# Optimization experiments

Hardware: AMD Instinct MI355X
Metric: run time of the kernel (lower is better)

## Reference

```python
import jax, jax.numpy as jnp
import numpy as np

H = 3          # num_hops + 1
N = 16384      # nodes per hop (seq len after view(1, -1, d))
D_MODEL = 256
D_STATE = 16
D_CONV = 8
EXPAND = 2
D_INNER = EXPAND * D_MODEL  # 512
DT_RANK = (D_MODEL + 15) // 16  # 16


def setup_inputs() -> dict:
    key = jax.random.key(0)
    ks = jax.random.split(key, 10)
    s = 0.02
    h = jax.random.normal(ks[0], (H, N, D_MODEL), jnp.float32)
    in_proj_w = jax.random.normal(ks[1], (H, 2 * D_INNER, D_MODEL), jnp.float32) * s
    conv_w = jax.random.normal(ks[2], (H, D_INNER, D_CONV), jnp.float32) * s
    conv_b = jax.random.normal(ks[3], (H, D_INNER), jnp.float32) * s
    x_proj_w = jax.random.normal(ks[4], (H, DT_RANK + 2 * D_STATE, D_INNER), jnp.float32) * s
    dt_proj_w = jax.random.normal(ks[5], (H, D_INNER, DT_RANK), jnp.float32) * s
    # dt bias so that softplus(dt_bias) is a small positive step (mamba-style init)
    dt_proj_b = jax.random.uniform(ks[6], (H, D_INNER), jnp.float32, minval=-5.0, maxval=-2.0)
    # A_log init: A = [1..d_state] broadcast over channels (S4D-real init)
    A_log = jnp.log(jnp.tile(jnp.arange(1, D_STATE + 1, dtype=jnp.float32), (H, D_INNER, 1)))
    D_skip = jnp.ones((H, D_INNER), jnp.float32)
    out_proj_w = jax.random.normal(ks[7], (H, D_MODEL, D_INNER), jnp.float32) * s
    return {
        "h": h, "in_proj_w": in_proj_w, "conv_w": conv_w, "conv_b": conv_b,
        "x_proj_w": x_proj_w, "dt_proj_w": dt_proj_w, "dt_proj_b": dt_proj_b,
        "A_log": A_log, "D_skip": D_skip, "out_proj_w": out_proj_w,
    }


def _mamba_one_hop(h, ipw, cw, cb, xpw, dtw, dtb, A_log, Dp, opw):
    # h: [N, d_model] -- seq len N, batch 1 (squeezed)
    xz = h @ ipw.T                              # [N, 2*d_inner]
    x, z = jnp.split(xz, 2, axis=-1)            # each [N, d_inner]
    # causal depthwise conv1d (left pad d_conv-1, truncate to N)
    xp = jnp.pad(x, ((D_CONV - 1, 0), (0, 0)))
    xc = cb + sum(cw[:, k] * xp[k:k + N] for k in range(D_CONV))  # [N, d_inner]
    u = jax.nn.silu(xc)
    # input-dependent dt, B, C
    x_dbl = u @ xpw.T                           # [N, dt_rank + 2*d_state]
    dt = x_dbl[:, :DT_RANK]
    Bm = x_dbl[:, DT_RANK:DT_RANK + D_STATE]    # [N, d_state]
    Cm = x_dbl[:, DT_RANK + D_STATE:]           # [N, d_state]
    delta = jax.nn.softplus(dt @ dtw.T + dtb)   # [N, d_inner]
    A = -jnp.exp(A_log)                         # [d_inner, d_state]

    def step(state, inp):
        d_t, b_t, c_t, u_t = inp                # [d_inner],[d_state],[d_state],[d_inner]
        dA = jnp.exp(d_t[:, None] * A)          # [d_inner, d_state]
        state = dA * state + (d_t * u_t)[:, None] * b_t[None, :]
        y_t = jnp.sum(state * c_t[None, :], axis=-1)  # [d_inner]
        return state, y_t

    state0 = jnp.zeros((D_INNER, D_STATE), h.dtype)
    _, y = jax.lax.scan(step, state0, (delta, Bm, Cm, u))  # y: [N, d_inner]
    y = y + u * Dp
    y = y * jax.nn.silu(z)
    return y @ opw.T                            # [N, d_model]


def reference(h, in_proj_w, conv_w, conv_b, x_proj_w, dt_proj_w, dt_proj_b,
              A_log, D_skip, out_proj_w):
    # vmap over the (num_hops+1) independent Mamba blocks
    return jax.vmap(_mamba_one_hop)(h, in_proj_w, conv_w, conv_b, x_proj_w,
                                    dt_proj_w, dt_proj_b, A_log, D_skip, out_proj_w)
```

## Files before the change

kernel.cpp:

```cpp
#include <hip/hip_runtime.h>

#define N_SEQ   16384
#define DM      256
#define DI      512
#define DS      16
#define DTR     16
#define NCHUNK  256
#define CHUNK   64
#define NSEG    8
#define SEGLEN  32

typedef short bf16x8 __attribute__((ext_vector_type(8)));
typedef float f32x4  __attribute__((ext_vector_type(4)));

__device__ __forceinline__ float b2f(ushort u){
  union { unsigned int i; float f; } v; v.i = ((unsigned int)u) << 16; return v.f;
}
__device__ __forceinline__ ushort f2b(float f){
  union { float f; unsigned int i; } v; v.f = f;
  unsigned int r = v.i + 0x7fffu + ((v.i >> 16) & 1u);
  return (ushort)(r >> 16);
}
__device__ __forceinline__ float silu_f(float x){
  return x * __builtin_amdgcn_rcpf(1.f + __expf(-x));
}
__device__ __forceinline__ void async16(const ushort* g, short* l){
  __builtin_amdgcn_global_load_lds(
      (const __attribute__((address_space(1))) unsigned int*)g,
      (__attribute__((address_space(3))) unsigned int*)l, 16, 0, 0);
}

__global__ __launch_bounds__(256) void cvt_kernel(const float* __restrict__ src,
                                                  ushort* __restrict__ dst, int n){
  int i = (blockIdx.x * 256 + threadIdx.x) * 4;
  if (i >= n) return;
  float4 v = *(const float4*)(src + i);
  ushort4 o;
  o.x = f2b(v.x); o.y = f2b(v.y); o.z = f2b(v.z); o.w = f2b(v.w);
  *(ushort4*)(dst + i) = o;
}

template<int BM, int BN, int WAR, int WWR, int MODE>
__global__ __launch_bounds__(256) void gemm2(const ushort* __restrict__ A,
                                             const ushort* __restrict__ W,
                                             int M, int Nn, int K,
                                             void* __restrict__ out0,
                                             void* __restrict__ out1, int ldc){
  constexpr int AI = WAR / 16, WI = WWR / 16;
  constexpr int WROWS = BM / WAR;
  constexpr int SMEM_STAGE = (BM + BN) * 64 * 2;
  constexpr int SMEM_EPI   = (MODE == 0) ? BM * (BN + 8) * 2 : 0;
  constexpr int SMEM = SMEM_STAGE > SMEM_EPI ? SMEM_STAGE : SMEM_EPI;
  __shared__ char smem[SMEM];
  short* As = (short*)smem;
  short* Ws = As + BM * 64;

  const int tid = threadIdx.x, lane = tid & 63, wid = tid >> 6;
  const int bz = blockIdx.z;
  const int rowBase = blockIdx.x * BM, colBase = blockIdx.y * BN;
  const ushort* Ah = A + (size_t)bz * M * K + (size_t)rowBase * K;
  const ushort* Wh = W + (size_t)bz * Nn * K + (size_t)colBase * K;
  const int wmi = wid % WROWS, wni = wid / WROWS;
  const int lr = lane & 15, q = lane >> 4;
  const int srow = lane >> 3, scg = lane & 7;

  f32x4 acc[AI][WI];
  #pragma unroll
  for (int ai = 0; ai < AI; ai++)
    #pragma unroll
    for (int wi = 0; wi < WI; wi++)
      acc[ai][wi] = (f32x4){0.f, 0.f, 0.f, 0.f};

  for (int kt = 0; kt < K; kt += 64){
    #pragma unroll
    for (int wdx = wid; wdx < BM / 8; wdx += 4){
      int r = wdx * 8 + srow;
      async16(Ah + (size_t)r * K + kt + ((scg ^ (r & 7)) * 8), As + wdx * 512);
    }
    #pragma unroll
    for (int wdx = wid; wdx < BN / 8; wdx += 4){
      int r = wdx * 8 + srow;
      async16(Wh + (size_t)r * K + kt + ((scg ^ (r & 7)) * 8), Ws + wdx * 512);
    }
    __syncthreads();
    #pragma unroll
    for (int ks = 0; ks < 64; ks += 32){
      bf16x8 wf[WI], af[AI];
      #pragma unroll
      for (int wi = 0; wi < WI; wi++){
        int row = wni * WWR + wi * 16 + lr;
        int pg = ((ks >> 3) + q) ^ (row & 7);
        wf[wi] = *(const bf16x8*)&Ws[row * 64 + pg * 8];
      }
      #pragma unroll
      for (int ai = 0; ai < AI; ai++){
        int row = wmi * WAR + ai * 16 + lr;
        int pg = ((ks >> 3) + q) ^ (row & 7);
        af[ai] = *(const bf16x8*)&As[row * 64 + pg * 8];
      }
      #pragma unroll
      for (int ai = 0; ai < AI; ai++)
        #pragma unroll
        for (int wi = 0; wi < WI; wi++)
          acc[ai][wi] = __builtin_amdgcn_mfma_f32_16x16x32_bf16(wf[wi], af[ai], acc[ai][wi], 0, 0, 0);
    }
    __syncthreads();
  }

  if (MODE == 0){
    const bool isz = (colBase >= DI);
    short* Cl = (short*)smem;
    constexpr int LDC = BN + 8;
    #pragma unroll
    for (int ai = 0; ai < AI; ai++){
      #pragma unroll
      for (int wi = 0; wi < WI; wi++){
        int trow = wmi * WAR + ai * 16 + lr;
        int tcol = wni * WWR + wi * 16 + q * 4;
        ushort4 pk;
        float v0 = acc[ai][wi][0], v1 = acc[ai][wi][1], v2 = acc[ai][wi][2], v3 = acc[ai][wi][3];
        if (isz){ v0 = silu_f(v0); v1 = silu_f(v1); v2 = silu_f(v2); v3 = silu_f(v3); }
        pk.x = f2b(v0); pk.y = f2b(v1); pk.z = f2b(v2); pk.w = f2b(v3);
        *(ushort4*)&Cl[trow * LDC + tcol] = pk;
      }
    }
    __syncthreads();
    ushort* dst = isz ? (ushort*)out1 : (ushort*)out0;
    const int colx = isz ? colBase - DI : colBase;
    const int rr = tid >> 4, ch = tid & 15;
    #pragma unroll
    for (int i = 0; i < BM / 16; i++){
      int trow = i * 16 + rr;
      uint4 v = *(uint4*)&Cl[trow * LDC + ch * 8];
      *(uint4*)(dst + ((size_t)bz * M + rowBase + trow) * DI + colx + ch * 8) = v;
    }
  } else {
    float* o = (float*)out0;
    #pragma unroll
    for (int ai = 0; ai < AI; ai++){
      #pragma unroll
      for (int wi = 0; wi < WI; wi++){
        int row = rowBase + wmi * WAR + ai * 16 + lr;
        int col = colBase + wni * WWR + wi * 16 + q * 4;
        *(float4*)&o[((size_t)bz * M + row) * ldc + col] = *(float4*)&acc[ai][wi];
      }
    }
  }
}

__global__ __launch_bounds__(256) void conv_kernel(const ushort* __restrict__ x_bf,
                                                   const float* __restrict__ cw,
                                                   const float* __restrict__ cb,
                                                   ushort* __restrict__ u_bf){
  const int SEG = 128;
  const int hop = blockIdx.z;
  const int c0 = threadIdx.x * 2;
  const int t0 = blockIdx.x * SEG;
  float k0[8], k1[8];
  {
    const float* r0 = cw + (size_t)(hop * DI + c0) * 8;
    float4 a = *(const float4*)r0, b = *(const float4*)(r0 + 4);
    k0[0]=a.x;k0[1]=a.y;k0[2]=a.z;k0[3]=a.w;k0[4]=b.x;k0[5]=b.y;k0[6]=b.z;k0[7]=b.w;
    float4 c = *(const float4*)(r0 + 8), d = *(const float4*)(r0 + 12);
    k1[0]=c.x;k1[1]=c.y;k1[2]=c.z;k1[3]=c.w;k1[4]=d.x;k1[5]=d.y;k1[6]=d.z;k1[7]=d.w;
  }
  float2 bias = *(const float2*)(cb + hop * DI + c0);
  const int rb = hop * N_SEQ;
  float w0[7], w1[7];
  #pragma unroll
  for (int j = 0; j < 7; j++){
    int t = t0 - 7 + j;
    if (t >= 0){
      ushort2 xv = *(const ushort2*)&x_bf[(size_t)(rb + t) * DI + c0];
      w0[j] = b2f(xv.x); w1[j] = b2f(xv.y);
    } else { w0[j] = 0.f; w1[j] = 0.f; }
  }
  #pragma unroll 4
  for (int tt = 0; tt < SEG; tt++){
    ushort2 xv = *(const ushort2*)&x_bf[(size_t)(rb + t0 + tt) * DI + c0];
    float x0 = b2f(xv.x), x1 = b2f(xv.y);
    float a0 = fmaf(k0[7], x0, bias.x), a1 = fmaf(k1[7], x1, bias.y);
    #pragma unroll
    for (int j = 0; j < 7; j++){ a0 = fmaf(k0[j], w0[j], a0); a1 = fmaf(k1[j], w1[j], a1); }
    ushort2 o; o.x = f2b(silu_f(a0)); o.y = f2b(silu_f(a1));
    *(ushort2*)&u_bf[(size_t)(rb + t0 + tt) * DI + c0] = o;
    #pragma unroll
    for (int j = 0; j < 6; j++){ w0[j] = w0[j + 1]; w1[j] = w1[j + 1]; }
    w0[6] = x0; w1[6] = x1;
  }
}

__global__ __launch_bounds__(256) void dtd_kernel(const float* __restrict__ xdbl,
                                                  const float* __restrict__ dtw,
                                                  const float* __restrict__ dtb,
                                                  ushort* __restrict__ delta_bf){
  const int TT = 64;
  const int hop = blockIdx.z;
  const int c = blockIdx.y * 256 + threadIdx.x;
  const int t0 = blockIdx.x * TT;
  float w0[16];
  {
    const float* wr = dtw + (size_t)(hop * DI + c) * DTR;
    #pragma unroll
    for (int r = 0; r < 16; r += 4){
      float4 v = *(const float4*)(wr + r);
      w0[r]=v.x; w0[r+1]=v.y; w0[r+2]=v.z; w0[r+3]=v.w;
    }
  }
  const float bias = dtb[hop * DI + c];
  #pragma unroll 2
  for (int tt = 0; tt < TT; tt++){
    const size_t row = (size_t)(hop * N_SEQ + t0 + tt);
    const float* xr = xdbl + row * 48;
    float a = bias;
    #pragma unroll
    for (int j = 0; j < 16; j++) a = fmaf(xr[j], w0[j], a);
    float t1 = __expf(a);
    float sp = (a > 20.f) ? a : __logf(1.f + t1);
    delta_bf[row * DI + c] = f2b(sp);
  }
}

__device__ __forceinline__ void state_update(float* st, float e1, float du, const float* bb){
  float p[16];
  p[0]=e1;        p[1]=p[0]*p[0]; p[2]=p[1]*p[0]; p[3]=p[1]*p[1];
  p[4]=p[3]*p[0]; p[5]=p[3]*p[1]; p[6]=p[3]*p[2]; p[7]=p[3]*p[3];
  p[8]=p[7]*p[0]; p[9]=p[7]*p[1]; p[10]=p[7]*p[2]; p[11]=p[7]*p[3];
  p[12]=p[7]*p[4]; p[13]=p[7]*p[5]; p[14]=p[7]*p[6]; p[15]=p[7]*p[7];
  #pragma unroll
  for (int s = 0; s < 16; s++) st[s] = fmaf(st[s], p[s], du * bb[s]);
}

__global__ __launch_bounds__(256) void scan1_kernel(const ushort* __restrict__ u_bf,
                                                    const ushort* __restrict__ delta_bf,
                                                    const float* __restrict__ xdbl,
                                                    float* __restrict__ qstate,
                                                    float* __restrict__ sdsum){
  const int g = blockIdx.x, hop = blockIdx.z;
  const int c = blockIdx.y * 256 + threadIdx.x;
  const int rowbase = hop * N_SEQ + g * CHUNK;
  float st[16];
  #pragma unroll
  for (int s = 0; s < 16; s++) st[s] = 0.f;
  float sd = 0.f;
  #pragma unroll 2
  for (int t = 0; t < CHUNK; t++){
    const size_t row = (size_t)(rowbase + t);
    const float* xr = xdbl + row * 48;
    float ld = b2f(delta_bf[row * DI + c]);
    float lu = b2f(u_bf[row * DI + c]);
    float e1 = __expf(-ld);
    sd += ld;
    state_update(st, e1, ld * lu, xr + 16);
  }
  const int gidx = hop * NCHUNK + g;
  sdsum[(size_t)gidx * DI + c] = sd;
  #pragma unroll
  for (int s = 0; s < 16; s++) qstate[((size_t)gidx * 16 + s) * DI + c] = st[s];
}

__global__ __launch_bounds__(256) void combineA(float* __restrict__ qstate,
                                                const float* __restrict__ sdsum,
                                                const float* __restrict__ A_log,
                                                float* __restrict__ segQ,
                                                float* __restrict__ segS){
  const int tid = threadIdx.x;
  const int seg = blockIdx.x >> 1;
  const int c = (blockIdx.x & 1) * 256 + tid;
  const int s = blockIdx.y, hop = blockIdx.z;
  const float a = -__expf(A_log[(size_t)(hop * DI + c) * DS + s]);
  float carry = 0.f, S = 0.f;
  for (int j = 0; j < SEGLEN; j++){
    const int gidx = hop * NCHUNK + seg * SEGLEN + j;
    const size_t idx = ((size_t)gidx * 16 + s) * DI + c;
    float q = qstate[idx];
    qstate[idx] = carry;
    float sdv = sdsum[(size_t)gidx * DI + c];
    S += sdv;
    carry = __expf(sdv * a) * carry + q;
  }
  const size_t chse = (((size_t)hop * DS + s) * NSEG + seg) * DI + c;
  segQ[chse] = carry;
  segS[chse] = S;
}

__global__ __launch_bounds__(256) void combineB(float* __restrict__ segQ,
                                                const float* __restrict__ segS,
                                                const float* __restrict__ A_log){
  const int c = blockIdx.x * 256 + threadIdx.x;
  const int s = blockIdx.y, hop = blockIdx.z;
  const float a = -__expf(A_log[(size_t)(hop * DI + c) * DS + s]);
  float carry = 0.f;
  #pragma unroll
  for (int seg = 0; seg < NSEG; seg++){
    const size_t i = (((size_t)hop * DS + s) * NSEG + seg) * DI + c;
    float q = segQ[i];
    segQ[i] = carry;
    carry = __expf(segS[i] * a) * carry + q;
  }
}

__global__ __launch_bounds__(256) void combineC(float* __restrict__ qstate,
                                                const float* __restrict__ sdsum,
                                                const float* __restrict__ A_log,
                                                const float* __restrict__ segC){
  const int tid = threadIdx.x;
  const int seg = blockIdx.x >> 1;
  const int c = (blockIdx.x & 1) * 256 + tid;
  const int s = blockIdx.y, hop = blockIdx.z;
  const float a = -__expf(A_log[(size_t)(hop * DI + c) * DS + s]);
  const float C0 = segC[(((size_t)hop * DS + s) * NSEG + seg) * DI + c];
  float cum = 0.f;
  for (int j = 0; j < SEGLEN; j++){
    const int gidx = hop * NCHUNK + seg * SEGLEN + j;
    const size_t idx = ((size_t)gidx * 16 + s) * DI + c;
    qstate[idx] += C0 * __expf(a * cum);
    cum += sdsum[(size_t)gidx * DI + c];
  }
}

__global__ __launch_bounds__(256) void scan2_kernel(const ushort* __restrict__ u_bf,
                                                    const ushort* __restrict__ delta_bf,
                                                    const float* __restrict__ xdbl,
                                                    const float* __restrict__ istate,
                                                    const ushort* __restrict__ szl_bf,
                                                    const float* __restrict__ Dskip,
                                                    ushort* __restrict__ yg){
  const int g = blockIdx.x, hop = blockIdx.z;
  const int c = blockIdx.y * 256 + threadIdx.x;
  const int rowbase = hop * N_SEQ + g * CHUNK;
  const int gidx = hop * NCHUNK + g;
  float st[16];
  #pragma unroll
  for (int s = 0; s < 16; s++) st[s] = istate[((size_t)gidx * 16 + s) * DI + c];
  const float Dc = Dskip[hop * DI + c];
  #pragma unroll 2
  for (int t = 0; t < CHUNK; t++){
    const size_t row = (size_t)(rowbase + t);
    const float* xr = xdbl + row * 48;
    float ld = b2f(delta_bf[row * DI + c]);
    float lu = b2f(u_bf[row * DI + c]);
    float e1 = __expf(-ld);
    state_update(st, e1, ld * lu, xr + 16);
    float y = lu * Dc;
    #pragma unroll
    for (int s = 0; s < 16; s++) y = fmaf(st[s], xr[32 + s], y);
    float sz = b2f(szl_bf[row * DI + c]);
    yg[row * DI + c] = f2b(y * sz);
  }
}

extern "C" void kernel_launch(void* const* d_in, const int* in_sizes, int n_in,
                              void* d_out, int out_size, void* d_ws, size_t ws_size,
                              hipStream_t stream) {
  const float* h     = (const float*)d_in[0];
  const float* ipw   = (const float*)d_in[1];
  const float* cw    = (const float*)d_in[2];
  const float* cb    = (const float*)d_in[3];
  const float* xpw   = (const float*)d_in[4];
  const float* dtw   = (const float*)d_in[5];
  const float* dtb   = (const float*)d_in[6];
  const float* A_log = (const float*)d_in[7];
  const float* Dsk   = (const float*)d_in[8];
  const float* opw   = (const float*)d_in[9];
  float* out = (float*)d_out;

  char* p = (char*)d_ws;
  auto alloc = [&](size_t bytes) -> void* {
    void* r = (void*)p; p += (bytes + 255) & ~(size_t)255; return r;
  };
  ushort* h_bf     = (ushort*)alloc((size_t)3 * N_SEQ * DM * 2);
  ushort* wip_bf   = (ushort*)alloc((size_t)3 * 1024 * DM * 2);
  ushort* wxp_bf   = (ushort*)alloc((size_t)3 * 48 * DI * 2);
  ushort* wop_bf   = (ushort*)alloc((size_t)3 * DM * DI * 2);
  ushort* x_bf     = (ushort*)alloc((size_t)3 * N_SEQ * DI * 2);
  ushort* szl_bf   = (ushort*)alloc((size_t)3 * N_SEQ * DI * 2);
  ushort* u_bf     = (ushort*)alloc((size_t)3 * N_SEQ * DI * 2);
  ushort* delta_bf = (ushort*)alloc((size_t)3 * N_SEQ * DI * 2);
  float*  xdbl     = (float*)alloc((size_t)3 * N_SEQ * 48 * 4);
  float*  qstate   = (float*)alloc((size_t)3 * NCHUNK * 16 * DI * 4);
  float*  sdsum    = (float*)alloc((size_t)3 * NCHUNK * DI * 4);
  float*  segQ     = (float*)alloc((size_t)3 * DS * NSEG * DI * 4);
  float*  segS     = (float*)alloc((size_t)3 * DS * NSEG * DI * 4);
  ushort* ygated   = x_bf;

  cvt_kernel<<<12288, 256, 0, stream>>>(h,   h_bf,   3 * N_SEQ * DM);
  cvt_kernel<<<768,   256, 0, stream>>>(ipw, wip_bf, 3 * 1024 * DM);
  cvt_kernel<<<72,    256, 0, stream>>>(xpw, wxp_bf, 3 * 48 * DI);
  cvt_kernel<<<384,   256, 0, stream>>>(opw, wop_bf, 3 * DM * DI);

  gemm2<128, 128, 64, 64, 0><<<dim3(128, 8, 3), 256, 0, stream>>>(
      h_bf, wip_bf, N_SEQ, 1024, DM, x_bf, szl_bf, 0);

  conv_kernel<<<dim3(128, 1, 3), 256, 0, stream>>>(x_bf, cw, cb, u_bf);

  gemm2<64, 48, 16, 48, 1><<<dim3(256, 1, 3), 256, 0, stream>>>(
      u_bf, wxp_bf, N_SEQ, 48, DI, xdbl, nullptr, 48);

  dtd_kernel<<<dim3(256, 2, 3), 256, 0, stream>>>(xdbl, dtw, dtb, delta_bf);

  scan1_kernel<<<dim3(NCHUNK, 2, 3), 256, 0, stream>>>(u_bf, delta_bf, xdbl, qstate, sdsum);
  combineA<<<dim3(16, 16, 3), 256, 0, stream>>>(qstate, sdsum, A_log, segQ, segS);
  combineB<<<dim3(2, 16, 3), 256, 0, stream>>>(segQ, segS, A_log);
  combineC<<<dim3(16, 16, 3), 256, 0, stream>>>(qstate, sdsum, A_log, segQ);
  scan2_kernel<<<dim3(NCHUNK, 2, 3), 256, 0, stream>>>(u_bf, delta_bf, xdbl, qstate, szl_bf, Dsk, ygated);

  gemm2<128, 128, 64, 64, 1><<<dim3(128, 2, 3), 256, 0, stream>>>(
      ygated, wop_bf, N_SEQ, DM, DI, out, nullptr, 256);
}
```

Measured before the change: 362.3 us.

## Fuse dt projection into scan1, merge conversions, fold combineB, two channels per thread

Merges the four fp32-to-bf16 conversion launches into a single launch and shrinks the conv segment length so the conv kernel gets four times as many blocks. The dt projection and softplus move into scan1, which now writes delta itself, and exp(-delta) is computed as 1/(1+exp(a)). combineB is removed and its serial segment carry is recomputed inside combineC. Scan kernels now handle two channels per thread with paired loads and stores, halving their grid. The goal is fewer launches and less delta traffic, at the cost of more registers and some redundant carry work in combineC.

```diff
diff --git a/kernel.cpp b/kernel.cpp
--- a/kernel.cpp
+++ b/kernel.cpp
@@ -30,14 +30,23 @@
       (__attribute__((address_space(3))) unsigned int*)l, 16, 0, 0);
 }
 
-__global__ __launch_bounds__(256) void cvt_kernel(const float* __restrict__ src,
-                                                  ushort* __restrict__ dst, int n){
-  int i = (blockIdx.x * 256 + threadIdx.x) * 4;
+__global__ __launch_bounds__(256) void cvt_all(const float* __restrict__ s0, ushort* __restrict__ d0, int n0,
+                                               const float* __restrict__ s1, ushort* __restrict__ d1, int n1,
+                                               const float* __restrict__ s2, ushort* __restrict__ d2, int n2,
+                                               const float* __restrict__ s3, ushort* __restrict__ d3, int n3,
+                                               int b0, int b1, int b2){
+  int b = blockIdx.x;
+  const float* s; ushort* d; int n, base;
+  if (b < b0)      { s = s0; d = d0; n = n0; base = b; }
+  else if (b < b1) { s = s1; d = d1; n = n1; base = b - b0; }
+  else if (b < b2) { s = s2; d = d2; n = n2; base = b - b1; }
+  else             { s = s3; d = d3; n = n3; base = b - b2; }
+  int i = (base * 256 + threadIdx.x) * 4;
   if (i >= n) return;
-  float4 v = *(const float4*)(src + i);
+  float4 v = *(const float4*)(s + i);
   ushort4 o;
   o.x = f2b(v.x); o.y = f2b(v.y); o.z = f2b(v.z); o.w = f2b(v.w);
-  *(ushort4*)(dst + i) = o;
+  *(ushort4*)(d + i) = o;
 }
 
 template<int BM, int BN, int WAR, int WWR, int MODE>
@@ -152,7 +161,7 @@
                                                    const float* __restrict__ cw,
                                                    const float* __restrict__ cb,
                                                    ushort* __restrict__ u_bf){
-  const int SEG = 128;
+  const int SEG = 32;
   const int hop = blockIdx.z;
   const int c0 = threadIdx.x * 2;
   const int t0 = blockIdx.x * SEG;
@@ -190,37 +199,6 @@
   }
 }
 
-__global__ __launch_bounds__(256) void dtd_kernel(const float* __restrict__ xdbl,
-                                                  const float* __restrict__ dtw,
-                                                  const float* __restrict__ dtb,
-                                                  ushort* __restrict__ delta_bf){
-  const int TT = 64;
-  const int hop = blockIdx.z;
-  const int c = blockIdx.y * 256 + threadIdx.x;
-  const int t0 = blockIdx.x * TT;
-  float w0[16];
-  {
-    const float* wr = dtw + (size_t)(hop * DI + c) * DTR;
-    #pragma unroll
-    for (int r = 0; r < 16; r += 4){
-      float4 v = *(const float4*)(wr + r);
-      w0[r]=v.x; w0[r+1]=v.y; w0[r+2]=v.z; w0[r+3]=v.w;
-    }
-  }
-  const float bias = dtb[hop * DI + c];
-  #pragma unroll 2
-  for (int tt = 0; tt < TT; tt++){
-    const size_t row = (size_t)(hop * N_SEQ + t0 + tt);
-    const float* xr = xdbl + row * 48;
-    float a = bias;
-    #pragma unroll
-    for (int j = 0; j < 16; j++) a = fmaf(xr[j], w0[j], a);
-    float t1 = __expf(a);
-    float sp = (a > 20.f) ? a : __logf(1.f + t1);
-    delta_bf[row * DI + c] = f2b(sp);
-  }
-}
-
 __device__ __forceinline__ void state_update(float* st, float e1, float du, const float* bb){
   float p[16];
   p[0]=e1;        p[1]=p[0]*p[0]; p[2]=p[1]*p[0]; p[3]=p[1]*p[1];
@@ -230,33 +208,64 @@
   #pragma unroll
   for (int s = 0; s < 16; s++) st[s] = fmaf(st[s], p[s], du * bb[s]);
 }
+__device__ __forceinline__ void delta_e1(float a, float& delta, float& e1){
+  float t1 = __expf(a);
+  e1 = __builtin_amdgcn_rcpf(1.f + t1);
+  delta = (a > 20.f) ? a : __logf(1.f + t1);
+}
 
 __global__ __launch_bounds__(256) void scan1_kernel(const ushort* __restrict__ u_bf,
-                                                    const ushort* __restrict__ delta_bf,
                                                     const float* __restrict__ xdbl,
+                                                    const float* __restrict__ dtw,
+                                                    const float* __restrict__ dtb,
+                                                    ushort* __restrict__ delta_bf,
                                                     float* __restrict__ qstate,
                                                     float* __restrict__ sdsum){
   const int g = blockIdx.x, hop = blockIdx.z;
-  const int c = blockIdx.y * 256 + threadIdx.x;
+  const int c0 = threadIdx.x * 2;
   const int rowbase = hop * N_SEQ + g * CHUNK;
-  float st[16];
-  #pragma unroll
-  for (int s = 0; s < 16; s++) st[s] = 0.f;
-  float sd = 0.f;
+  float wa[16], wb[16];
+  {
+    const float* wr = dtw + (size_t)(hop * DI + c0) * DTR;
+    #pragma unroll
+    for (int r = 0; r < 16; r += 4){
+      float4 va = *(const float4*)(wr + r);
+      wa[r]=va.x; wa[r+1]=va.y; wa[r+2]=va.z; wa[r+3]=va.w;
+      float4 vb = *(const float4*)(wr + DTR + r);
+      wb[r]=vb.x; wb[r+1]=vb.y; wb[r+2]=vb.z; wb[r+3]=vb.w;
+    }
+  }
+  const float2 bias = *(const float2*)(dtb + hop * DI + c0);
+  float sta[16], stb[16];
+  #pragma unroll
+  for (int s = 0; s < 16; s++){ sta[s] = 0.f; stb[s] = 0.f; }
+  float sda = 0.f, sdb = 0.f;
   #pragma unroll 2
   for (int t = 0; t < CHUNK; t++){
     const size_t row = (size_t)(rowbase + t);
     const float* xr = xdbl + row * 48;
-    float ld = b2f(delta_bf[row * DI + c]);
-    float lu = b2f(u_bf[row * DI + c]);
-    float e1 = __expf(-ld);
-    sd += ld;
-    state_update(st, e1, ld * lu, xr + 16);
+    ushort2 u2 = *(const ushort2*)&u_bf[row * DI + c0];
+    float ua = b2f(u2.x), ub = b2f(u2.y);
+    float aa = bias.x, ab = bias.y;
+    #pragma unroll
+    for (int j = 0; j < 16; j++){ aa = fmaf(xr[j], wa[j], aa); ab = fmaf(xr[j], wb[j], ab); }
+    float da, e1a, db, e1b;
+    delta_e1(aa, da, e1a);
+    delta_e1(ab, db, e1b);
+    ushort2 d2; d2.x = f2b(da); d2.y = f2b(db);
+    *(ushort2*)&delta_bf[row * DI + c0] = d2;
+    sda += da; sdb += db;
+    state_update(sta, e1a, da * ua, xr + 16);
+    state_update(stb, e1b, db * ub, xr + 16);
   }
   const int gidx = hop * NCHUNK + g;
-  sdsum[(size_t)gidx * DI + c] = sd;
-  #pragma unroll
-  for (int s = 0; s < 16; s++) qstate[((size_t)gidx * 16 + s) * DI + c] = st[s];
+  float2 sd2; sd2.x = sda; sd2.y = sdb;
+  *(float2*)&sdsum[(size_t)gidx * DI + c0] = sd2;
+  #pragma unroll
+  for (int s = 0; s < 16; s++){
+    float2 q2; q2.x = sta[s]; q2.y = stb[s];
+    *(float2*)&qstate[((size_t)gidx * 16 + s) * DI + c0] = q2;
+  }
 }
 
 __global__ __launch_bounds__(256) void combineA(float* __restrict__ qstate,
@@ -284,37 +293,26 @@
   segS[chse] = S;
 }
 
-__global__ __launch_bounds__(256) void combineB(float* __restrict__ segQ,
-                                                const float* __restrict__ segS,
-                                                const float* __restrict__ A_log){
-  const int c = blockIdx.x * 256 + threadIdx.x;
-  const int s = blockIdx.y, hop = blockIdx.z;
-  const float a = -__expf(A_log[(size_t)(hop * DI + c) * DS + s]);
-  float carry = 0.f;
-  #pragma unroll
-  for (int seg = 0; seg < NSEG; seg++){
-    const size_t i = (((size_t)hop * DS + s) * NSEG + seg) * DI + c;
-    float q = segQ[i];
-    segQ[i] = carry;
-    carry = __expf(segS[i] * a) * carry + q;
-  }
-}
-
 __global__ __launch_bounds__(256) void combineC(float* __restrict__ qstate,
                                                 const float* __restrict__ sdsum,
                                                 const float* __restrict__ A_log,
-                                                const float* __restrict__ segC){
+                                                const float* __restrict__ segQ,
+                                                const float* __restrict__ segS){
   const int tid = threadIdx.x;
   const int seg = blockIdx.x >> 1;
   const int c = (blockIdx.x & 1) * 256 + tid;
   const int s = blockIdx.y, hop = blockIdx.z;
   const float a = -__expf(A_log[(size_t)(hop * DI + c) * DS + s]);
-  const float C0 = segC[(((size_t)hop * DS + s) * NSEG + seg) * DI + c];
+  float carry = 0.f;
+  for (int sg = 0; sg < seg; sg++){
+    const size_t i = (((size_t)hop * DS + s) * NSEG + sg) * DI + c;
+    carry = __expf(segS[i] * a) * carry + segQ[i];
+  }
   float cum = 0.f;
   for (int j = 0; j < SEGLEN; j++){
     const int gidx = hop * NCHUNK + seg * SEGLEN + j;
     const size_t idx = ((size_t)gidx * 16 + s) * DI + c;
-    qstate[idx] += C0 * __expf(a * cum);
+    qstate[idx] = fmaf(carry, __expf(a * cum), qstate[idx]);
     cum += sdsum[(size_t)gidx * DI + c];
   }
 }
@@ -327,26 +325,33 @@
                                                     const float* __restrict__ Dskip,
                                                     ushort* __restrict__ yg){
   const int g = blockIdx.x, hop = blockIdx.z;
-  const int c = blockIdx.y * 256 + threadIdx.x;
+  const int c0 = threadIdx.x * 2;
   const int rowbase = hop * N_SEQ + g * CHUNK;
   const int gidx = hop * NCHUNK + g;
-  float st[16];
-  #pragma unroll
-  for (int s = 0; s < 16; s++) st[s] = istate[((size_t)gidx * 16 + s) * DI + c];
-  const float Dc = Dskip[hop * DI + c];
+  float sta[16], stb[16];
+  #pragma unroll
+  for (int s = 0; s < 16; s++){
+    float2 q2 = *(const float2*)&istate[((size_t)gidx * 16 + s) * DI + c0];
+    sta[s] = q2.x; stb[s] = q2.y;
+  }
+  const float2 Dc = *(const float2*)(Dskip + hop * DI + c0);
   #pragma unroll 2
   for (int t = 0; t < CHUNK; t++){
     const size_t row = (size_t)(rowbase + t);
     const float* xr = xdbl + row * 48;
-    float ld = b2f(delta_bf[row * DI + c]);
-    float lu = b2f(u_bf[row * DI + c]);
-    float e1 = __expf(-ld);
-    state_update(st, e1, ld * lu, xr + 16);
-    float y = lu * Dc;
-    #pragma unroll
-    for (int s = 0; s < 16; s++) y = fmaf(st[s], xr[32 + s], y);
-    float sz = b2f(szl_bf[row * DI + c]);
-    yg[row * DI + c] = f2b(y * sz);
+    ushort2 d2 = *(const ushort2*)&delta_bf[row * DI + c0];
+    ushort2 u2 = *(const ushort2*)&u_bf[row * DI + c0];
+    ushort2 z2 = *(const ushort2*)&szl_bf[row * DI + c0];
+    float da = b2f(d2.x), db = b2f(d2.y);
+    float ua = b2f(u2.x), ub = b2f(u2.y);
+    float e1a = __expf(-da), e1b = __expf(-db);
+    state_update(sta, e1a, da * ua, xr + 16);
+    state_update(stb, e1b, db * ub, xr + 16);
+    float ya = ua * Dc.x, yb = ub * Dc.y;
+    #pragma unroll
+    for (int s = 0; s < 16; s++){ ya = fmaf(sta[s], xr[32 + s], ya); yb = fmaf(stb[s], xr[32 + s], yb); }
+    ushort2 o; o.x = f2b(ya * b2f(z2.x)); o.y = f2b(yb * b2f(z2.y));
+    *(ushort2*)&yg[row * DI + c0] = o;
   }
 }
 
@@ -384,26 +389,24 @@
   float*  segS     = (float*)alloc((size_t)3 * DS * NSEG * DI * 4);
   ushort* ygated   = x_bf;
 
-  cvt_kernel<<<12288, 256, 0, stream>>>(h,   h_bf,   3 * N_SEQ * DM);
-  cvt_kernel<<<768,   256, 0, stream>>>(ipw, wip_bf, 3 * 1024 * DM);
-  cvt_kernel<<<72,    256, 0, stream>>>(xpw, wxp_bf, 3 * 48 * DI);
-  cvt_kernel<<<384,   256, 0, stream>>>(opw, wop_bf, 3 * DM * DI);
+  const int n0 = 3 * N_SEQ * DM, n1 = 3 * 1024 * DM, n2 = 3 * 48 * DI, n3 = 3 * DM * DI;
+  const int nb0 = n0 / 1024, nb1 = n1 / 1024, nb2 = n2 / 1024, nb3 = n3 / 1024;
+  cvt_all<<<nb0 + nb1 + nb2 + nb3, 256, 0, stream>>>(
+      h, h_bf, n0, ipw, wip_bf, n1, xpw, wxp_bf, n2, opw, wop_bf, n3,
+      nb0, nb0 + nb1, nb0 + nb1 + nb2);
 
   gemm2<128, 128, 64, 64, 0><<<dim3(128, 8, 3), 256, 0, stream>>>(
       h_bf, wip_bf, N_SEQ, 1024, DM, x_bf, szl_bf, 0);
 
-  conv_kernel<<<dim3(128, 1, 3), 256, 0, stream>>>(x_bf, cw, cb, u_bf);
+  conv_kernel<<<dim3(512, 1, 3), 256, 0, stream>>>(x_bf, cw, cb, u_bf);
 
   gemm2<64, 48, 16, 48, 1><<<dim3(256, 1, 3), 256, 0, stream>>>(
       u_bf, wxp_bf, N_SEQ, 48, DI, xdbl, nullptr, 48);
 
-  dtd_kernel<<<dim3(256, 2, 3), 256, 0, stream>>>(xdbl, dtw, dtb, delta_bf);
-
-  scan1_kernel<<<dim3(NCHUNK, 2, 3), 256, 0, stream>>>(u_bf, delta_bf, xdbl, qstate, sdsum);
+  scan1_kernel<<<dim3(NCHUNK, 1, 3), 256, 0, stream>>>(u_bf, xdbl, dtw, dtb, delta_bf, qstate, sdsum);
   combineA<<<dim3(16, 16, 3), 256, 0, stream>>>(qstate, sdsum, A_log, segQ, segS);
-  combineB<<<dim3(2, 16, 3), 256, 0, stream>>>(segQ, segS, A_log);
-  combineC<<<dim3(16, 16, 3), 256, 0, stream>>>(qstate, sdsum, A_log, segQ);
-  scan2_kernel<<<dim3(NCHUNK, 2, 3), 256, 0, stream>>>(u_bf, delta_bf, xdbl, qstate, szl_bf, Dsk, ygated);
+  combineC<<<dim3(16, 16, 3), 256, 0, stream>>>(qstate, sdsum, A_log, segQ, segS);
+  scan2_kernel<<<dim3(NCHUNK, 1, 3), 256, 0, stream>>>(u_bf, delta_bf, xdbl, qstate, szl_bf, Dsk, ygated);
 
   gemm2<128, 128, 64, 64, 1><<<dim3(128, 2, 3), 256, 0, stream>>>(
       ygated, wop_bf, N_SEQ, DM, DI, out, nullptr, 256);
```

After: 350.7 us. -3.2%, faster.
